# Performance work log

Measured on AMD Instinct MI355X. Metric: run time of the kernel, lower is better.

Reference implementation:

```python
import jax, jax.numpy as jnp
from jax import lax
import numpy as np


def hac_round(X, W):
    """Avg-linkage HAC build+cut rounding of fractional SDP matrix X (D,D).
    Returns the 0/1 symmetric round_matrix with 1-diagonal."""
    D = X.shape[0]
    dt = X.dtype
    MAXD = jnp.max(jnp.abs(X)) * 1000.0  # _MAX_DIST sentinel
    max_sim = jnp.max(X)                 # max_similarity passed by forward()
    tril_mask = jnp.tril(jnp.ones((D, D), dtype=bool))
    # use_similarities=True branch: Y = MAXD*tril + (max_sim - X).triu(1)
    Y = jnp.where(tril_mask, MAXD, max_sim - X)
    values = jnp.min(Y, axis=1)
    indices = jnp.argmin(Y, axis=1)
    parents = jnp.arange(2 * D - 1)
    p2i = jnp.arange(2 * D - 1)   # parent_to_idx
    i2p = jnp.arange(D)           # idx_to_parent
    cs = jnp.ones(2 * D - 1, dtype=dt)
    energy = jnp.zeros(2 * D - 1, dtype=dt)
    clustering = jnp.zeros((2 * D - 1, D), dtype=dt)
    clustering = clustering.at[jnp.arange(D), jnp.arange(D)].set(jnp.arange(1, D + 1, dtype=dt))
    R = jnp.eye(D, dtype=dt)

    def body(i, st):
        Y, values, indices, parents, p2i, i2p, cs, energy, clustering, R = st
        max_node = D + i
        m1 = jnp.argmin(values)
        m2 = indices[m1]
        p1 = i2p[p2i[i2p[m1]]]
        p2 = i2p[p2i[i2p[m2]]]
        parents = parents.at[p1].set(max_node).at[p2].set(max_node)
        i2p = i2p.at[m1].set(max_node)
        p2i = p2i.at[max_node].set(m1)
        max_mask = Y == MAXD
        cs1, cs2 = cs[p1], cs[p2]
        ncs = cs1 + cs2
        cs = cs.at[max_node].set(ncs)
        # weighted average-linkage merged distances
        newv = (jnp.minimum(Y[m1, :], Y[:, m1]) * cs1 + jnp.minimum(Y[:, m2], Y[m2, :]) * cs2) / ncs
        Y = Y.at[:, m1].set(newv).at[m1, :].set(newv)
        Y = jnp.where(max_mask, MAXD, Y)
        Y = Y.at[:, m2].set(MAXD).at[m2, :].set(MAXD)
        values = values.at[m2].set(MAXD)
        vmask = values == MAXD
        values = jnp.where(vmask, MAXD, jnp.min(Y, axis=1))
        indices = jnp.argmin(Y, axis=1)
        # cut decision for the new internal node
        crow = clustering[p1] + clustering[p2]
        leaf = crow > 0                      # membership of new cluster
        lf = leaf.astype(dt)
        merge_e = lf @ (W @ lf)              # sum of W over leaf x leaf pairs
        e_sum = energy[p1] + energy[p2]
        take = merge_e >= e_sum
        energy = energy.at[max_node].set(jnp.where(take, merge_e, e_sum))
        crow = jnp.where(take & leaf, (max_node).astype(dt), crow)
        clustering = clustering.at[max_node].set(crow)
        R = jnp.where(take & (leaf[:, None] & leaf[None, :]), jnp.asarray(1.0, dt), R)
        return (Y, values, indices, parents, p2i, i2p, cs, energy, clustering, R)

    st = (Y, values, indices, parents, p2i, i2p, cs, energy, clustering, R)
    st = lax.fori_loop(0, D - 1, body, st)
    return st[-1]


def setup_inputs() -> dict:
    key = jax.random.key(0)
    k1, k2 = jax.random.split(key)
    D = 1024
    A = jax.random.uniform(k1, (D, D), dtype=jnp.float32)
    X = 0.5 * (A + A.T)                      # symmetric fractional decisions
    X = X.at[jnp.arange(D), jnp.arange(D)].set(1.0)  # 1-diagonal
    W = jnp.triu(jax.random.normal(k2, (D, D), dtype=jnp.float32), 1)  # triu(1) weights
    return {"X": X, "W": W}


def reference(X, W):
    # straight-through estimator: hard rounded solution, identity gradient w.r.t. X
    R = hac_round(X, W)
    return X + lax.stop_gradient(R - X)
```

## Files before the change

### kernel.cpp

```cpp
#include <hip/hip_runtime.h>
#include <stdint.h>

#define D 1024

typedef unsigned long long u64;
typedef unsigned int u32;

__device__ __forceinline__ u32 enc_f(float f) {
    u32 b = __float_as_uint(f);
    return (b & 0x80000000u) ? ~b : (b | 0x80000000u);
}
__device__ __forceinline__ float dec_f(u32 u) {
    u32 b = (u & 0x80000000u) ? (u ^ 0x80000000u) : ~u;
    return __uint_as_float(b);
}

__device__ __forceinline__ void barrier_lds_only() {
    __builtin_amdgcn_sched_barrier(0);
    asm volatile("s_waitcnt lgkmcnt(0)" ::: "memory");
    __builtin_amdgcn_s_barrier();
    asm volatile("" ::: "memory");
    __builtin_amdgcn_sched_barrier(0);
}

__global__ void k_maxred(const float* __restrict__ X, u32* scal) {
    float mx = -INFINITY, ma = 0.f;
    int stride = gridDim.x * blockDim.x;
    for (int i = blockIdx.x * blockDim.x + threadIdx.x; i < D * D; i += stride) {
        float v = X[i];
        mx = fmaxf(mx, v);
        ma = fmaxf(ma, fabsf(v));
    }
    for (int o = 32; o; o >>= 1) {
        mx = fmaxf(mx, __shfl_xor(mx, o));
        ma = fmaxf(ma, __shfl_xor(ma, o));
    }
    if ((threadIdx.x & 63) == 0) {
        atomicMax(&scal[0], enc_f(mx));
        atomicMax(&scal[1], enc_f(ma));
    }
}

__global__ void k_init(const float* __restrict__ X, const float* __restrict__ W,
                       float2* __restrict__ dc, const u32* __restrict__ scal) {
    int idx = blockIdx.x * blockDim.x + threadIdx.x;
    if (idx >= D * D) return;
    float max_sim = dec_f(scal[0]);
    float MAXD = __fmul_rn(dec_f(scal[1]), 1000.0f);
    int i = idx >> 10, j = idx & (D - 1);
    float x = X[idx];
    float di = (i == j) ? MAXD : __fsub_rn(max_sim, x);
    float cx = (i == j) ? 0.0f : (W[idx] + W[j * D + i]);
    dc[idx] = make_float2(di, cx);
}

__global__ void k_rowmin(const float2* __restrict__ dc, float* __restrict__ values_g,
                         int* __restrict__ indices_g, const u32* __restrict__ scal) {
    int r = blockIdx.x;
    int lane = threadIdx.x;
    float MAXD = __fmul_rn(dec_f(scal[1]), 1000.0f);
    u64 best = ((u64)__float_as_uint(MAXD) << 32);
    const float4* row4 = (const float4*)(dc + (size_t)r * D);
    for (int c = lane; c < D / 2; c += 64) {
        float4 q = row4[c];
        int j0 = c << 1;
        if (j0 > r) {
            u64 k = ((u64)__float_as_uint(q.x) << 32) | (u32)j0;
            if (k < best) best = k;
        }
        if (j0 + 1 > r) {
            u64 k = ((u64)__float_as_uint(q.z) << 32) | (u32)(j0 + 1);
            if (k < best) best = k;
        }
    }
    for (int o = 32; o; o >>= 1) {
        u64 k2 = __shfl_xor(best, o);
        if (k2 < best) best = k2;
    }
    if (lane == 0) {
        values_g[r] = __uint_as_float((u32)(best >> 32));
        indices_g[r] = (int)(best & 0xffffffffu);
    }
}

__global__ void __launch_bounds__(1024) k_hac(
        float2* __restrict__ dc,
        const float* __restrict__ values_g, const int* __restrict__ indices_g,
        int* __restrict__ labels_g, const u32* __restrict__ scal) {
    __shared__ __align__(16) float values_l[D];
    __shared__ float values_stage[D];
    __shared__ int indices_l[D];
    __shared__ __align__(16) float newv_h[2][D];
    __shared__ __align__(16) float crossv_h[2][D];
    __shared__ float cs_l[D];
    __shared__ unsigned char dead_l[D];
    __shared__ unsigned char marked_l[D];
    __shared__ int slot_l[D];
    __shared__ int label_l[D];
    __shared__ double within_l[D];
    __shared__ double energy_l[D];
    __shared__ int rlist[2][D];
    __shared__ int nrec[2];
    __shared__ u64 s_best[2];
    __shared__ float s_cross12;
    __shared__ int s_takeP, s_m1P, s_labP;

    const int t = threadIdx.x;
    const int lane = t & 63, wid = t >> 6;
    const float MAXD = __fmul_rn(dec_f(scal[1]), 1000.0f);
    const u32 MAXDb = __float_as_uint(MAXD);

    values_l[t] = values_g[t];
    indices_l[t] = indices_g[t];
    cs_l[t] = 1.0f;
    dead_l[t] = 0;
    marked_l[t] = 0;
    slot_l[t] = t;
    label_l[t] = t;
    within_l[t] = 0.0;
    energy_l[t] = 0.0;
    if (t == 0) {
        s_takeP = 0; s_m1P = -1; s_labP = 0;
        nrec[0] = 0; nrec[1] = 0;
        s_best[0] = ~0ull; s_best[1] = ~0ull;
    }
    __syncthreads();
    {
        u64 key = ((u64)__float_as_uint(values_l[t]) << 32) | ((u32)t << 10) |
                  (u32)indices_l[t];
        for (int o = 32; o; o >>= 1) {
            u64 k2 = __shfl_xor(key, o);
            if (k2 < key) key = k2;
        }
        if (lane == 0) atomicMin(&s_best[0], key);
    }
    __syncthreads();

    for (int it = 0; it < D - 1; ++it) {
        const int cb = it & 1, pb = cb ^ 1;

        const u64 bk = s_best[cb];
        const int m1 = (int)((bk >> 10) & 1023);
        const int m2 = (int)(bk & 1023);
        const float cs1 = cs_l[m1], cs2 = cs_l[m2];
        const float ncs = __fadd_rn(cs1, cs2);
        const int pm1 = s_m1P;
        const int takeP = s_takeP, labP = s_labP;
        if (t == 0) s_best[pb] = ~0ull;

        if (marked_l[t]) { values_l[t] = values_stage[t]; marked_l[t] = 0; }
        if (t == m2) {
            dead_l[m2] = 1;
            values_l[m2] = MAXD;
            indices_l[m2] = 0;
        }
        const bool alive = !dead_l[t];

        const bool h1 = (m1 == pm1), h2 = (m2 == pm1);

        float2 v1 = make_float2(0.f, 0.f), v2 = make_float2(0.f, 0.f);
        if (alive || t == m2) {
            if (!h1) v1 = dc[(size_t)m1 * D + t];
            if (!h2) v2 = dc[(size_t)m2 * D + t];
        }
        float d1, c1, d2, c2;
        if (h1) { d1 = newv_h[pb][t]; c1 = crossv_h[pb][t]; }
        else    { d1 = v1.x;          c1 = v1.y; }
        if (h2) { d2 = newv_h[pb][t]; c2 = crossv_h[pb][t]; }
        else    { d2 = v2.x;          c2 = v2.y; }

        {
            int sl = slot_l[t];
            if (takeP && sl == pm1) label_l[t] = labP;
            if (sl == m2) slot_l[t] = m1;
        }

        float nv = MAXD, ncx = 0.0f;
        bool do_st = false;
        if (t == m2) s_cross12 = c1;
        if (alive && t != m1) {
            nv = __fdiv_rn(__fadd_rn(__fmul_rn(d1, cs1), __fmul_rn(d2, cs2)), ncs);
            ncx = c1 + c2;
            dc[(size_t)m1 * D + t] = make_float2(nv, ncx);
            do_st = true;
        }
        newv_h[cb][t] = nv;
        crossv_h[cb][t] = ncx;

        {
            float v = values_l[t];
            if (t == m1) {
                values_l[t] = MAXD;
                marked_l[t] = 1;
            } else if (alive && v < MAXD) {
                int idx = indices_l[t];
                if (idx == m2) {
                    rlist[cb][atomicAdd(&nrec[cb], 1)] = t;
                    values_l[t] = MAXD;
                    marked_l[t] = 1;
                } else if (idx == m1) {
                    if (nv <= v) values_l[t] = nv;
                    else {
                        rlist[cb][atomicAdd(&nrec[cb], 1)] = t;
                        values_l[t] = MAXD;
                        marked_l[t] = 1;
                    }
                } else if (t < m1) {
                    if (nv < v) { values_l[t] = nv; indices_l[t] = m1; }
                    else if (nv == v && m1 < idx) indices_l[t] = m1;
                }
            }
        }
        barrier_lds_only();

        if (t == m1) cs_l[m1] = ncs;
        const int n = nrec[cb];
        if (t == 0) nrec[pb] = 0;

        if (wid == 0) {
            if (do_st) dc[(size_t)t * D + m1] = make_float2(nv, ncx);
            if (lane == 0) {
                double merge_e = within_l[m1] + within_l[m2] + (double)s_cross12;
                double e_sum = energy_l[m1] + energy_l[m2];
                int take = (merge_e >= e_sum) ? 1 : 0;
                within_l[m1] = merge_e;
                energy_l[m1] = take ? merge_e : e_sum;
                s_takeP = take;
                s_m1P = m1;
                s_labP = D + it;
            }
            const float4* v4 = (const float4*)values_l;
            u64 bb = ~0ull;
#pragma unroll
            for (int c = 0; c < 4; ++c) {
                int fi = lane + 64 * c;
                float4 q = v4[fi];
                int b = fi << 2;
                u64 k;
                k = ((u64)__float_as_uint(q.x) << 32) | (u32)(b + 0); if (k < bb) bb = k;
                k = ((u64)__float_as_uint(q.y) << 32) | (u32)(b + 1); if (k < bb) bb = k;
                k = ((u64)__float_as_uint(q.z) << 32) | (u32)(b + 2); if (k < bb) bb = k;
                k = ((u64)__float_as_uint(q.w) << 32) | (u32)(b + 3); if (k < bb) bb = k;
            }
            for (int o = 32; o; o >>= 1) {
                u64 k2 = __shfl_xor(bb, o);
                if (k2 < bb) bb = k2;
            }
            if (lane == 0) {
                int r = (int)(bb & 1023);
                int idx = indices_l[r];
                atomicMin(&s_best[pb],
                          (bb & 0xffffffff00000000ull) | ((u32)r << 10) | (u32)idx);
            }
        } else if (wid == 1) {
            if (do_st) dc[(size_t)t * D + m1] = make_float2(nv, ncx);
            u64 bb = ((u64)MAXDb << 32);
            const float4* nv4 = (const float4*)newv_h[cb];
            for (int c = lane; c < D / 4; c += 64) {
                float4 q = nv4[c];
                int j0 = c << 2;
#pragma unroll
                for (int e = 0; e < 4; ++e) {
                    int j = j0 + e;
                    float dv = (e == 0) ? q.x : (e == 1) ? q.y : (e == 2) ? q.z : q.w;
                    if (j > m1) {
                        u64 k = ((u64)__float_as_uint(dv) << 32) | (u32)j;
                        if (k < bb) bb = k;
                    }
                }
            }
            for (int o = 32; o; o >>= 1) {
                u64 k2 = __shfl_xor(bb, o);
                if (k2 < bb) bb = k2;
            }
            if (lane == 0) {
                values_stage[m1] = __uint_as_float((u32)(bb >> 32));
                indices_l[m1] = (int)(bb & 0xffffffffu);
                atomicMin(&s_best[pb],
                          (bb & 0xffffffff00000000ull) | ((u32)m1 << 10) | (bb & 1023));
            }
        } else {
            bool pend_st = do_st;
            for (int q = wid - 2; q < n; q += 14) {
                const int r = rlist[cb][q];
                const float subst = newv_h[cb][r];
                const float4* row4 = (const float4*)(dc + (size_t)r * D);
                float4 a0 = row4[lane];
                float4 a1 = row4[lane + 64];
                float4 a2 = row4[lane + 128];
                float4 a3 = row4[lane + 192];
                float4 a4 = row4[lane + 256];
                float4 a5 = row4[lane + 320];
                float4 a6 = row4[lane + 384];
                float4 a7 = row4[lane + 448];
                if (pend_st) {
                    dc[(size_t)t * D + m1] = make_float2(nv, ncx);
                    pend_st = false;
                }
                u64 bb = ((u64)MAXDb << 32);
#define ACC2(af, koff)                                                          \
                {                                                               \
                    int j0 = (lane + (koff)) << 1;                              \
                    float dv0 = (j0 == m1) ? subst : (af).x;                    \
                    if (j0 > r && !dead_l[j0]) {                                \
                        u64 k = ((u64)__float_as_uint(dv0) << 32) | (u32)j0;    \
                        if (k < bb) bb = k;                                     \
                    }                                                           \
                    int j1 = j0 + 1;                                            \
                    float dv1 = (j1 == m1) ? subst : (af).z;                    \
                    if (j1 > r && !dead_l[j1]) {                                \
                        u64 k = ((u64)__float_as_uint(dv1) << 32) | (u32)j1;    \
                        if (k < bb) bb = k;                                     \
                    }                                                           \
                }
                ACC2(a0, 0)
                ACC2(a1, 64)
                ACC2(a2, 128)
                ACC2(a3, 192)
                ACC2(a4, 256)
                ACC2(a5, 320)
                ACC2(a6, 384)
                ACC2(a7, 448)
#undef ACC2
                for (int o = 32; o; o >>= 1) {
                    u64 k2 = __shfl_xor(bb, o);
                    if (k2 < bb) bb = k2;
                }
                if (lane == 0) {
                    values_stage[r] = __uint_as_float((u32)(bb >> 32));
                    indices_l[r] = (int)(bb & 0xffffffffu);
                    atomicMin(&s_best[pb],
                              (bb & 0xffffffff00000000ull) | ((u32)r << 10) | (bb & 1023));
                }
            }
            if (pend_st) dc[(size_t)t * D + m1] = make_float2(nv, ncx);
        }
        __syncthreads();
    }

    {
        int lab = label_l[t];
        if (s_takeP && slot_l[t] == s_m1P) lab = s_labP;
        labels_g[t] = lab;
    }
}

__global__ void k_out(const int* __restrict__ labels, float* __restrict__ out) {
    int idx = blockIdx.x * blockDim.x + threadIdx.x;
    if (idx >= D * D) return;
    int i = idx >> 10, j = idx & (D - 1);
    out[idx] = (i == j || labels[i] == labels[j]) ? 1.0f : 0.0f;
}

extern "C" void kernel_launch(void* const* d_in, const int* in_sizes, int n_in,
                              void* d_out, int out_size, void* d_ws, size_t ws_size,
                              hipStream_t stream) {
    const float* X = (const float*)d_in[0];
    const float* W = (const float*)d_in[1];

    char* ws = (char*)d_ws;
    const size_t MAT_BYTES = (size_t)D * D * sizeof(float);
    float2* dc = (float2*)ws;
    float* values_g = (float*)(ws + 2 * MAT_BYTES);
    int* indices_g = (int*)(ws + 2 * MAT_BYTES + 4096);
    int* labels_g = (int*)(ws + 2 * MAT_BYTES + 8192);
    u32* scal = (u32*)(ws + 2 * MAT_BYTES + 12288);

    hipMemsetAsync(scal, 0, 2 * sizeof(u32), stream);
    k_maxred<<<256, 256, 0, stream>>>(X, scal);
    k_init<<<(D * D) / 256, 256, 0, stream>>>(X, W, dc, scal);
    k_rowmin<<<D, 64, 0, stream>>>(dc, values_g, indices_g, scal);
    k_hac<<<1, 1024, 0, stream>>>(dc, values_g, indices_g, labels_g, scal);
    k_out<<<(D * D) / 256, 256, 0, stream>>>(labels_g, (float*)d_out);
}
```

Before: 3.203 ms.

## Speculatively prefetch next iteration's merge rows before the loop barrier

At the end of each merge iteration, each thread reads the current best (m1, m2) candidate from s_best and prefetches the dc entries for those rows before the barrier. If the next iteration's final pair matches the prediction, it uses the prefetched values and skips the dependent global load at the top of the loop. Otherwise it falls back to fresh loads. It also changes how previous-iteration newv values are patched in, and now loads even for dead threads. The trade is extra speculative global reads in exchange for taking load latency off the serial critical path. There is a correctness risk because the prefetch reads s_best before all atomics and stores have completed.

```diff
diff --git a/kernel.cpp b/kernel.cpp
--- a/kernel.cpp
+++ b/kernel.cpp
@@ -136,12 +136,22 @@
     }
     __syncthreads();
 
+    int rp_s = -1, ip_s = -1;
+    float2 spec1 = make_float2(0.f, 0.f), spec2 = make_float2(0.f, 0.f);
+
     for (int it = 0; it < D - 1; ++it) {
         const int cb = it & 1, pb = cb ^ 1;
 
         const u64 bk = s_best[cb];
         const int m1 = (int)((bk >> 10) & 1023);
         const int m2 = (int)(bk & 1023);
+
+        const bool hit1 = (m1 == rp_s);
+        const bool hit2 = (m2 == ip_s);
+        float2 v1, v2;
+        if (hit1) v1 = spec1; else v1 = dc[(size_t)m1 * D + t];
+        if (hit2) v2 = spec2; else v2 = dc[(size_t)m2 * D + t];
+
         const float cs1 = cs_l[m1], cs2 = cs_l[m2];
         const float ncs = __fadd_rn(cs1, cs2);
         const int pm1 = s_m1P;
@@ -156,18 +166,15 @@
         }
         const bool alive = !dead_l[t];
 
-        const bool h1 = (m1 == pm1), h2 = (m2 == pm1);
-
-        float2 v1 = make_float2(0.f, 0.f), v2 = make_float2(0.f, 0.f);
-        if (alive || t == m2) {
-            if (!h1) v1 = dc[(size_t)m1 * D + t];
-            if (!h2) v2 = dc[(size_t)m2 * D + t];
-        }
-        float d1, c1, d2, c2;
-        if (h1) { d1 = newv_h[pb][t]; c1 = crossv_h[pb][t]; }
-        else    { d1 = v1.x;          c1 = v1.y; }
-        if (h2) { d2 = newv_h[pb][t]; c2 = crossv_h[pb][t]; }
-        else    { d2 = v2.x;          c2 = v2.y; }
+        float d1 = v1.x, c1 = v1.y, d2 = v2.x, c2 = v2.y;
+        if (hit1) {
+            if (m1 == pm1)     { d1 = newv_h[pb][t];  c1 = crossv_h[pb][t];  }
+            else if (t == pm1) { d1 = newv_h[pb][m1]; c1 = crossv_h[pb][m1]; }
+        }
+        if (hit2) {
+            if (m2 == pm1)     { d2 = newv_h[pb][t];  c2 = crossv_h[pb][t];  }
+            else if (t == pm1) { d2 = newv_h[pb][m2]; c2 = crossv_h[pb][m2]; }
+        }
 
         {
             int sl = slot_l[t];
@@ -335,6 +342,14 @@
             }
             if (pend_st) dc[(size_t)t * D + m1] = make_float2(nv, ncx);
         }
+
+        {
+            const u64 pred = s_best[pb];
+            rp_s = (int)((pred >> 10) & 1023);
+            ip_s = (int)(pred & 1023);
+            spec1 = dc[(size_t)rp_s * D + t];
+            spec2 = dc[(size_t)ip_s * D + t];
+        }
         __syncthreads();
     }
 
```

Measured after the change: 3.285 ms. 1.03x slower.
